# Kernel optimization log

Hardware: AMD Instinct MI355X
Metric: run time of the kernel (lower is better)

Reference implementation:

```python
import jax, jax.numpy as jnp
import numpy as np

EPS = 1e-5


def _rmsnorm(x, eps=EPS):
    return x * jax.lax.rsqrt(jnp.mean(x * x, axis=-1, keepdims=True) + eps)


def _bitlinear(x, w):
    # fla-style BitLinear: RMSNorm (no affine) -> 8-bit activation quant (STE)
    # -> ternary weight quant (STE) -> linear. w is [out, in].
    xn = _rmsnorm(x)
    s = 127.0 / jnp.clip(jnp.max(jnp.abs(xn), axis=-1, keepdims=True), 1e-5, None)
    xq = jnp.clip(jnp.round(xn * s), -128.0, 127.0) / s
    xq = xn + jax.lax.stop_gradient(xq - xn)
    ws = 1.0 / jnp.clip(jnp.mean(jnp.abs(w)), 1e-5, None)
    wq = jnp.clip(jnp.round(w * ws), -1.0, 1.0) / ws
    wq = w + jax.lax.stop_gradient(wq - w)
    return jnp.einsum('bld,od->blo', xq, wq)


def _hgrn_scan(i, f):
    # h_t = f_t * h_{t-1} + i_t along axis=2 (seq), h_0 = 0.
    def combine(a, b):
        fa, ia = a
        fb, ib = b
        return fa * fb, ia * fb + ib
    _, h = jax.lax.associative_scan(combine, (f, i), axis=2)
    return h


def _forward(hidden_states, Wi, Wf, Wg, Wo, g_norm_weight, num_heads=1):
    b, l, d = hidden_states.shape
    i = _bitlinear(hidden_states, Wi)
    f = jax.nn.sigmoid(_bitlinear(hidden_states, Wf))
    i = jax.nn.silu(i) * (1.0 - f)  # swiglu(i, 1-f)
    # [b, l, (h d)] -> [b, h, l, d_head]
    i = i.reshape(b, l, num_heads, -1).transpose(0, 2, 1, 3)
    f = f.reshape(b, l, num_heads, -1).transpose(0, 2, 1, 3)
    h = _hgrn_scan(i, f)
    h = h.transpose(0, 2, 1, 3).reshape(b, l, d)
    # FusedRMSNormSwishGate: rmsnorm(g)*weight * h*sigmoid(h)
    g = _bitlinear(hidden_states, Wg)
    o = _rmsnorm(g) * g_norm_weight * (h * jax.nn.sigmoid(h))
    return _bitlinear(o, Wo)


def setup_inputs() -> dict:
    key = jax.random.key(0)
    ks = jax.random.split(key, 5)
    B, L, D = 4, 2048, 2048
    gain = 2 ** (-2.5) * (6.0 / (2 * D)) ** 0.5  # xavier_uniform with gain 2^-2.5
    def w(k):
        return jax.random.uniform(k, (D, D), jnp.float32, -gain, gain)
    return {
        'hidden_states': jax.random.normal(ks[0], (B, L, D), jnp.float32),
        'Wi': w(ks[1]),
        'Wf': w(ks[2]),
        'Wg': w(ks[3]),
        'Wo': w(ks[4]),
        'g_norm_weight': jnp.ones((D,), jnp.float32),
    }


def reference(hidden_states, Wi, Wf, Wg, Wo, g_norm_weight):
    return _forward(hidden_states, Wi, Wf, Wg, Wo, g_norm_weight)
```

## Files before the change

### kernel.cpp

```cpp
#include <hip/hip_runtime.h>
#include <stdint.h>

#define B_DIM 4
#define L_DIM 2048
#define D_DIM 2048
#define M_DIM 8192
#define K_DIM 2048
#define N_DIM 2048
#define WELEM (D_DIM * D_DIM)
#define CHUNK 32
#define NCH (L_DIM / CHUNK)

typedef int v4i  __attribute__((ext_vector_type(4)));
typedef int v16i __attribute__((ext_vector_type(16)));
typedef unsigned short bfraw;

#define AS1 __attribute__((address_space(1)))
#define AS3 __attribute__((address_space(3)))

__device__ __forceinline__ void gl_lds16(const void* g, void* l) {
    __builtin_amdgcn_global_load_lds((AS1 void*)g, (AS3 void*)l, 16, 0, 0);
}

__device__ __forceinline__ void wg_barrier() {
    asm volatile("" ::: "memory");
    __builtin_amdgcn_s_barrier();
    asm volatile("" ::: "memory");
}

__device__ __forceinline__ float sigmoidf_(float x) { return 1.0f / (1.0f + expf(-x)); }

__device__ __forceinline__ float bf2f(bfraw u) {
    union { unsigned int i; float f; } c; c.i = ((unsigned int)u) << 16; return c.f;
}
__device__ __forceinline__ bfraw f2bf(float f) {
    union { float f; unsigned int i; } c; c.f = f;
    unsigned int lsb = (c.i >> 16) & 1;
    c.i += 0x7fffu + lsb;
    return (bfraw)(c.i >> 16);
}

__device__ __forceinline__ void store_out(float* p, float v) { *p = v; }
__device__ __forceinline__ void store_out(bfraw* p, float v) { *p = f2bf(v); }

__device__ __forceinline__ float block_sum256(float v) {
#pragma unroll
    for (int off = 32; off > 0; off >>= 1) v += __shfl_down(v, off);
    __shared__ float sb[4];
    int lane = threadIdx.x & 63, wv = threadIdx.x >> 6;
    __syncthreads();
    if (lane == 0) sb[wv] = v;
    __syncthreads();
    return sb[0] + sb[1] + sb[2] + sb[3];
}

__device__ __forceinline__ void block_sum_max256(float& s, float& m) {
#pragma unroll
    for (int off = 32; off > 0; off >>= 1) {
        s += __shfl_down(s, off);
        m = fmaxf(m, __shfl_down(m, off));
    }
    __shared__ float sb2[8];
    int lane = threadIdx.x & 63, wv = threadIdx.x >> 6;
    __syncthreads();
    if (lane == 0) { sb2[wv] = s; sb2[4 + wv] = m; }
    __syncthreads();
    s = sb2[0] + sb2[1] + sb2[2] + sb2[3];
    m = fmaxf(fmaxf(sb2[4], sb2[5]), fmaxf(sb2[6], sb2[7]));
}

__global__ void wstats1(const float* __restrict__ w0, const float* __restrict__ w1,
                        const float* __restrict__ w2, const float* __restrict__ w3,
                        float* __restrict__ wpart) {
    int w = blockIdx.x >> 7;
    int slice = blockIdx.x & 127;
    const float* W = (w == 0) ? w0 : ((w == 1) ? w1 : ((w == 2) ? w2 : w3));
    const float4* p = (const float4*)(W + (size_t)slice * (WELEM / 128));
    float s = 0.f;
    for (int i = threadIdx.x; i < (WELEM / 128 / 4); i += 256) {
        float4 v = p[i];
        s += fabsf(v.x) + fabsf(v.y) + fabsf(v.z) + fabsf(v.w);
    }
    s = block_sum256(s);
    if (threadIdx.x == 0) wpart[blockIdx.x] = s;
}

__global__ void wstats2(const float* __restrict__ wpart, float* __restrict__ wdeq) {
    int w = threadIdx.x >> 6;
    int lane = threadIdx.x & 63;
    float s = wpart[w * 128 + lane] + wpart[w * 128 + 64 + lane];
#pragma unroll
    for (int off = 32; off > 0; off >>= 1) s += __shfl_down(s, off);
    if (lane == 0) wdeq[w] = fmaxf(s * (1.0f / (float)WELEM), 1e-5f);
}

__global__ void quant_all(const float* __restrict__ w0, const float* __restrict__ w1,
                          const float* __restrict__ w2, const float* __restrict__ w3,
                          const float* __restrict__ wdeq, int8_t* __restrict__ wq,
                          const float* __restrict__ x, int8_t* __restrict__ xq,
                          float* __restrict__ adeq) {
    if (blockIdx.x < 16384) {
        size_t idx = (size_t)blockIdx.x * 256 + threadIdx.x;
        int w = (int)(idx >> 20);
        size_t g = idx & ((1u << 20) - 1);
        const float* W = (w == 0) ? w0 : ((w == 1) ? w1 : ((w == 2) ? w2 : w3));
        float inv = 1.0f / wdeq[w];
        float4 v = ((const float4*)W)[g];
        int q0 = (int)rintf(v.x * inv); q0 = q0 < -1 ? -1 : (q0 > 1 ? 1 : q0);
        int q1 = (int)rintf(v.y * inv); q1 = q1 < -1 ? -1 : (q1 > 1 ? 1 : q1);
        int q2 = (int)rintf(v.z * inv); q2 = q2 < -1 ? -1 : (q2 > 1 ? 1 : q2);
        int q3 = (int)rintf(v.w * inv); q3 = q3 < -1 ? -1 : (q3 > 1 ? 1 : q3);
        uint32_t p = (uint32_t)(q0 & 0xff) | ((uint32_t)(q1 & 0xff) << 8) |
                     ((uint32_t)(q2 & 0xff) << 16) | ((uint32_t)(q3 & 0xff) << 24);
        ((uint32_t*)(wq + (size_t)w * WELEM))[g] = p;
        return;
    }
    int row = blockIdx.x - 16384, tid = threadIdx.x;
    const float4* xr = (const float4*)(x + (size_t)row * D_DIM);
    float4 a = xr[2 * tid], b = xr[2 * tid + 1];
    float v[8] = {a.x, a.y, a.z, a.w, b.x, b.y, b.z, b.w};
    float ss = 0.f, mx = 0.f;
#pragma unroll
    for (int j = 0; j < 8; j++) { ss += v[j] * v[j]; mx = fmaxf(mx, fabsf(v[j])); }
    block_sum_max256(ss, mx);
    float inv = rsqrtf(ss * (1.0f / (float)D_DIM) + 1e-5f);
    float anc = fmaxf(mx * inv, 1e-5f);
    float s = 127.0f / anc;
    if (tid == 0) adeq[row] = anc * (1.0f / 127.0f);
    float sc = inv * s;
    int q[8];
#pragma unroll
    for (int j = 0; j < 8; j++) {
        int t = (int)rintf(v[j] * sc);
        q[j] = t < -128 ? -128 : (t > 127 ? 127 : t);
    }
    uint32_t lo = (uint32_t)(q[0] & 0xff) | ((uint32_t)(q[1] & 0xff) << 8) |
                  ((uint32_t)(q[2] & 0xff) << 16) | ((uint32_t)(q[3] & 0xff) << 24);
    uint32_t hi = (uint32_t)(q[4] & 0xff) | ((uint32_t)(q[5] & 0xff) << 8) |
                  ((uint32_t)(q[6] & 0xff) << 16) | ((uint32_t)(q[7] & 0xff) << 24);
    ((uint2*)(xq + (size_t)row * D_DIM))[tid] = make_uint2(lo, hi);
}

#define BM2 256
#define BN2 256
#define BKB 64
#define NT (K_DIM / BKB)

#define MFMA32(a, b, c) __builtin_amdgcn_mfma_i32_32x32x32_i8((a), (b), (c), 0, 0, 0)

template <typename OutT>
__device__ __forceinline__ void gemm_core(
    const int8_t* __restrict__ A, const int8_t* __restrict__ Bw,
    const float* __restrict__ adeq, float wsc,
    int m0, int n0, OutT* __restrict__ Cout) {
    __shared__ __align__(16) int8_t sA[4][BM2 * BKB];
    __shared__ __align__(16) int8_t sB[4][BN2 * BKB];
    int lane = threadIdx.x & 63;
    int wv = threadIdx.x >> 6;
    int wr = wv >> 2, wc = wv & 3;
    int r32 = lane & 31;
    int h32 = lane >> 5;
    const int ag = wr * 4;
    const int bg = wc * 2;
    const int lb = lane * 16;

    const v16i vzero = {0, 0, 0, 0, 0, 0, 0, 0, 0, 0, 0, 0, 0, 0, 0, 0};
    v16i acc[4][2];
#pragma unroll
    for (int m = 0; m < 4; m++)
#pragma unroll
        for (int n = 0; n < 2; n++) acc[m][n] = vzero;

    const int8_t* Asrc = A + (size_t)(m0 + r32) * K_DIM + h32 * 16;
    const int8_t* Bsrc = Bw + (size_t)(n0 + r32) * K_DIM + h32 * 16;

#define STG(c, kt) do {                                                                     \
    gl_lds16(Asrc + (size_t)(wv * 32) * K_DIM + (kt),      &sA[c][wv * 2048]);              \
    gl_lds16(Asrc + (size_t)(wv * 32) * K_DIM + (kt) + 32, &sA[c][wv * 2048 + 1024]);       \
    gl_lds16(Bsrc + (size_t)(wv * 32) * K_DIM + (kt),      &sB[c][wv * 2048]);              \
    gl_lds16(Bsrc + (size_t)(wv * 32) * K_DIM + (kt) + 32, &sB[c][wv * 2048 + 1024]);       \
  } while (0)

#define LDF(buf, grp, s) (*(const v4i*)(&(buf)[(grp) * 2048 + (s) * 1024 + lb]))

    STG(0, 0);
    STG(1, BKB);
    asm volatile("s_waitcnt vmcnt(4)" ::: "memory");
    wg_barrier();

    for (int t = 0; t < NT; ++t) {
        int cur = t & 3;
        const int8_t* bA = &sA[cur][0];
        const int8_t* bB = &sB[cur][0];

        v4i af[4][2], bf[2][2];
#pragma unroll
        for (int m = 0; m < 4; m++) {
            af[m][0] = LDF(bA, ag + m, 0);
            af[m][1] = LDF(bA, ag + m, 1);
        }
#pragma unroll
        for (int n = 0; n < 2; n++) {
            bf[n][0] = LDF(bB, bg + n, 0);
            bf[n][1] = LDF(bB, bg + n, 1);
        }

        if (t + 2 < NT) STG((t + 2) & 3, (t + 2) * BKB);

        __builtin_amdgcn_s_setprio(1);
#pragma unroll
        for (int s = 0; s < 2; s++)
#pragma unroll
            for (int m = 0; m < 4; m++)
#pragma unroll
                for (int n = 0; n < 2; n++)
                    acc[m][n] = MFMA32(af[m][s], bf[n][s], acc[m][n]);
        __builtin_amdgcn_s_setprio(0);

        if (t + 1 < NT) {
            if (t + 2 < NT)
                asm volatile("s_waitcnt vmcnt(4)" ::: "memory");
            else
                asm volatile("s_waitcnt vmcnt(0)" ::: "memory");
            wg_barrier();
        }
    }
#undef LDF
#undef STG

#pragma unroll
    for (int m = 0; m < 4; m++) {
#pragma unroll
        for (int r = 0; r < 16; r++) {
            int rr = (r & 3) + 8 * (r >> 2) + 4 * h32;
            int row = m0 + (ag + m) * 32 + rr;
            float rs = adeq[row] * wsc;
            OutT* crow = Cout + (size_t)row * N_DIM + n0 + bg * 32 + r32;
            store_out(crow,      (float)acc[m][0][r] * rs);
            store_out(crow + 32, (float)acc[m][1][r] * rs);
        }
    }
}

__global__ __launch_bounds__(512, 2) void gemm_ifg(
    const int8_t* __restrict__ xq, const int8_t* __restrict__ wq,
    const float* __restrict__ adeq, const float* __restrict__ wdeq,
    bfraw* __restrict__ bufI, bfraw* __restrict__ bufF, bfraw* __restrict__ bufG) {
    int widx = blockIdx.x >> 3;
    int n0 = (blockIdx.x & 7) * BN2;
    int m0 = blockIdx.y * BM2;
    bfraw* outp = (widx == 0) ? bufI : ((widx == 1) ? bufF : bufG);
    gemm_core<bfraw>(xq, wq + (size_t)widx * WELEM, adeq, wdeq[widx], m0, n0, outp);
}

__global__ __launch_bounds__(512, 2) void gemm_o(
    const int8_t* __restrict__ oq, const int8_t* __restrict__ wq,
    const float* __restrict__ odeq, const float* __restrict__ wdeq,
    float* __restrict__ out) {
    gemm_core<float>(oq, wq + 3 * (size_t)WELEM, odeq, wdeq[3], blockIdx.y * BM2,
                     blockIdx.x * BN2, out);
}

__global__ void scan1(const bfraw* __restrict__ iL, const bfraw* __restrict__ fL,
                      float* __restrict__ Fc, float* __restrict__ Ic) {
    int idx = blockIdx.x * 256 + threadIdx.x;
    int d = idx & (D_DIM - 1);
    int c = (idx >> 11) & (NCH - 1);
    int b = idx >> 17;
    size_t base = ((size_t)(b * L_DIM + c * CHUNK)) * D_DIM + d;
    float F = 1.f, h = 0.f;
#pragma unroll 4
    for (int t = 0; t < CHUNK; t++) {
        float fr = bf2f(fL[base + (size_t)t * D_DIM]);
        float ir = bf2f(iL[base + (size_t)t * D_DIM]);
        float fv = sigmoidf_(fr);
        float iv = ir * sigmoidf_(ir) * (1.0f - fv);
        h = fv * h + iv;
        F *= fv;
    }
    size_t ci = ((size_t)b * NCH + c) * D_DIM + d;
    Fc[ci] = F;
    Ic[ci] = h;
}

__global__ void scan2(const float* __restrict__ Fc, const float* __restrict__ Ic,
                      float* __restrict__ Hc) {
    int idx = blockIdx.x * 256 + threadIdx.x;
    int d = idx & (D_DIM - 1);
    int b = idx >> 11;
    float h = 0.f;
    for (int c0 = 0; c0 < NCH; c0 += 8) {
        float F[8], I[8];
#pragma unroll
        for (int j = 0; j < 8; j++) {
            size_t ci = ((size_t)b * NCH + c0 + j) * D_DIM + d;
            F[j] = Fc[ci];
            I[j] = Ic[ci];
        }
#pragma unroll
        for (int j = 0; j < 8; j++) {
            size_t ci = ((size_t)b * NCH + c0 + j) * D_DIM + d;
            Hc[ci] = h;
            h = F[j] * h + I[j];
        }
    }
}

__global__ void scan3(const bfraw* __restrict__ iL, const bfraw* __restrict__ fL,
                      const float* __restrict__ Hc, bfraw* __restrict__ hout) {
    int idx = blockIdx.x * 256 + threadIdx.x;
    int d = idx & (D_DIM - 1);
    int c = (idx >> 11) & (NCH - 1);
    int b = idx >> 17;
    size_t base = ((size_t)(b * L_DIM + c * CHUNK)) * D_DIM + d;
    float h = Hc[((size_t)b * NCH + c) * D_DIM + d];
#pragma unroll 4
    for (int t = 0; t < CHUNK; t++) {
        size_t a = base + (size_t)t * D_DIM;
        float fr = bf2f(fL[a]);
        float ir = bf2f(iL[a]);
        float fv = sigmoidf_(fr);
        float iv = ir * sigmoidf_(ir) * (1.0f - fv);
        h = fv * h + iv;
        hout[a] = f2bf(h);
    }
}

union BF8 { uint4 u; bfraw s[8]; };

__global__ void gout_quant(const bfraw* __restrict__ gL, const bfraw* __restrict__ h,
                           const float* __restrict__ gw, int8_t* __restrict__ oq,
                           float* __restrict__ odeq) {
    int row = blockIdx.x, tid = threadIdx.x;
    BF8 g8, h8;
    g8.u = ((const uint4*)(gL + (size_t)row * D_DIM))[tid];
    float gv[8];
    float ss = 0.f;
#pragma unroll
    for (int j = 0; j < 8; j++) { gv[j] = bf2f(g8.s[j]); ss += gv[j] * gv[j]; }
    float ssg = block_sum256(ss);
    float invg = rsqrtf(ssg * (1.0f / (float)D_DIM) + 1e-5f);

    h8.u = ((const uint4*)(h + (size_t)row * D_DIM))[tid];
    const float4* wr = (const float4*)gw;
    float4 w0 = wr[2 * tid], w1 = wr[2 * tid + 1];
    float wv[8] = {w0.x, w0.y, w0.z, w0.w, w1.x, w1.y, w1.z, w1.w};
    float o[8];
    float sso = 0.f, amax = 0.f;
#pragma unroll
    for (int j = 0; j < 8; j++) {
        float hv = bf2f(h8.s[j]);
        o[j] = gv[j] * invg * wv[j] * hv * sigmoidf_(hv);
        sso += o[j] * o[j];
        amax = fmaxf(amax, fabsf(o[j]));
    }
    block_sum_max256(sso, amax);
    float invo = rsqrtf(sso * (1.0f / (float)D_DIM) + 1e-5f);
    float anc = fmaxf(amax * invo, 1e-5f);
    float s = 127.0f / anc;
    if (tid == 0) odeq[row] = anc * (1.0f / 127.0f);
    float sc = invo * s;
    int q[8];
#pragma unroll
    for (int j = 0; j < 8; j++) {
        int t = (int)rintf(o[j] * sc);
        q[j] = t < -128 ? -128 : (t > 127 ? 127 : t);
    }
    uint32_t lo = (uint32_t)(q[0] & 0xff) | ((uint32_t)(q[1] & 0xff) << 8) |
                  ((uint32_t)(q[2] & 0xff) << 16) | ((uint32_t)(q[3] & 0xff) << 24);
    uint32_t hi = (uint32_t)(q[4] & 0xff) | ((uint32_t)(q[5] & 0xff) << 8) |
                  ((uint32_t)(q[6] & 0xff) << 16) | ((uint32_t)(q[7] & 0xff) << 24);
    ((uint2*)(oq + (size_t)row * D_DIM))[tid] = make_uint2(lo, hi);
}

extern "C" void kernel_launch(void* const* d_in, const int* in_sizes, int n_in,
                              void* d_out, int out_size, void* d_ws, size_t ws_size,
                              hipStream_t stream) {
    const float* x  = (const float*)d_in[0];
    const float* Wi = (const float*)d_in[1];
    const float* Wf = (const float*)d_in[2];
    const float* Wg = (const float*)d_in[3];
    const float* Wo = (const float*)d_in[4];
    const float* gw = (const float*)d_in[5];
    float* out = (float*)d_out;

    char* ws = (char*)d_ws;
    float*  wdeq  = (float*)(ws + 0);
    float*  wpart = (float*)(ws + 256);
    float*  adeq  = (float*)(ws + 0x10000);
    float*  odeq  = (float*)(ws + 0x20000);
    int8_t* xq    = (int8_t*)(ws + 0x100000);
    int8_t* wq    = (int8_t*)(ws + 0x1100000);
    float*  Fc    = (float*)(ws + 0x2100000);
    float*  Ic    = (float*)(ws + 0x2300000);
    float*  Hc    = (float*)(ws + 0x2500000);
    bfraw*  bufI  = (bfraw*)(ws + 0x4000000);
    bfraw*  bufF  = (bfraw*)(ws + 0x6000000);
    bfraw*  bufG  = (bfraw*)(ws + 0x8000000);
    bfraw*  hbuf  = (bfraw*)(ws + 0xA000000);

    wstats1<<<512, 256, 0, stream>>>(Wi, Wf, Wg, Wo, wpart);
    wstats2<<<1, 256, 0, stream>>>(wpart, wdeq);
    quant_all<<<16384 + 8192, 256, 0, stream>>>(Wi, Wf, Wg, Wo, wdeq, wq, x, xq, adeq);

    gemm_ifg<<<dim3(24, M_DIM / BM2), 512, 0, stream>>>(xq, wq, adeq, wdeq, bufI, bufF, bufG);

    scan1<<<2048, 256, 0, stream>>>(bufI, bufF, Fc, Ic);
    scan2<<<32, 256, 0, stream>>>(Fc, Ic, Hc);
    scan3<<<2048, 256, 0, stream>>>(bufI, bufF, Hc, hbuf);

    gout_quant<<<M_DIM, 256, 0, stream>>>(bufG, hbuf, gw, xq , odeq);
    gemm_o<<<dim3(N_DIM / BN2, M_DIM / BM2), 512, 0, stream>>>(xq , wq, odeq, wdeq, out);

    (void)in_sizes; (void)n_in; (void)out_size; (void)ws_size;
}
```

Baseline: 418.7 us.

## Software-pipeline LDS fragment loads against MFMA in int8 GEMM loop

Splits each K-tile into two halves held in separate register sets. The loads for the second half and for the next tile's first half are now issued while the MFMAs on the other half run, so LDS latency hides behind matrix math. The global prefetch is now issued at the top of the iteration. The wait before the barrier tightens from vmcnt(4) to vmcnt(0), which shrinks the effective global-load lookahead and may expose memory latency. It also uses more registers.

```diff
diff --git a/kernel.cpp b/kernel.cpp
--- a/kernel.cpp
+++ b/kernel.cpp
@@ -183,45 +183,54 @@
 
 #define LDF(buf, grp, s) (*(const v4i*)(&(buf)[(grp) * 2048 + (s) * 1024 + lb]))
 
+    v4i pa[4], pb[2];
+    v4i qa[4], qb[2];
+
     STG(0, 0);
     STG(1, BKB);
-    asm volatile("s_waitcnt vmcnt(4)" ::: "memory");
+    asm volatile("s_waitcnt vmcnt(0)" ::: "memory");
     wg_barrier();
+    pb[0] = LDF(sB[0], bg + 0, 0);
+    pb[1] = LDF(sB[0], bg + 1, 0);
+#pragma unroll
+    for (int m = 0; m < 4; m++) pa[m] = LDF(sA[0], ag + m, 0);
 
     for (int t = 0; t < NT; ++t) {
         int cur = t & 3;
-        const int8_t* bA = &sA[cur][0];
-        const int8_t* bB = &sB[cur][0];
-
-        v4i af[4][2], bf[2][2];
+        int nxt = (t + 1) & 3;
+
+        if (t + 2 < NT) STG((t + 2) & 3, (t + 2) * BKB);
+
+        qb[0] = LDF(sB[cur], bg + 0, 1);
+        qb[1] = LDF(sB[cur], bg + 1, 1);
+#pragma unroll
+        for (int m = 0; m < 4; m++) qa[m] = LDF(sA[cur], ag + m, 1);
+
+        __builtin_amdgcn_s_setprio(1);
 #pragma unroll
         for (int m = 0; m < 4; m++) {
-            af[m][0] = LDF(bA, ag + m, 0);
-            af[m][1] = LDF(bA, ag + m, 1);
-        }
-#pragma unroll
-        for (int n = 0; n < 2; n++) {
-            bf[n][0] = LDF(bB, bg + n, 0);
-            bf[n][1] = LDF(bB, bg + n, 1);
-        }
-
-        if (t + 2 < NT) STG((t + 2) & 3, (t + 2) * BKB);
+            acc[m][0] = MFMA32(pa[m], pb[0], acc[m][0]);
+            acc[m][1] = MFMA32(pa[m], pb[1], acc[m][1]);
+        }
+        __builtin_amdgcn_s_setprio(0);
+
+        if (t + 1 < NT) {
+            pb[0] = LDF(sB[nxt], bg + 0, 0);
+            pb[1] = LDF(sB[nxt], bg + 1, 0);
+#pragma unroll
+            for (int m = 0; m < 4; m++) pa[m] = LDF(sA[nxt], ag + m, 0);
+        }
 
         __builtin_amdgcn_s_setprio(1);
 #pragma unroll
-        for (int s = 0; s < 2; s++)
-#pragma unroll
-            for (int m = 0; m < 4; m++)
-#pragma unroll
-                for (int n = 0; n < 2; n++)
-                    acc[m][n] = MFMA32(af[m][s], bf[n][s], acc[m][n]);
+        for (int m = 0; m < 4; m++) {
+            acc[m][0] = MFMA32(qa[m], qb[0], acc[m][0]);
+            acc[m][1] = MFMA32(qa[m], qb[1], acc[m][1]);
+        }
         __builtin_amdgcn_s_setprio(0);
 
         if (t + 1 < NT) {
-            if (t + 2 < NT)
-                asm volatile("s_waitcnt vmcnt(4)" ::: "memory");
-            else
-                asm volatile("s_waitcnt vmcnt(0)" ::: "memory");
+            asm volatile("s_waitcnt vmcnt(0)" ::: "memory");
             wg_barrier();
         }
     }
```

New measurement: 490.5 us. 17.2% more time.
